# Kernel optimization log

Hardware: AMD Instinct MI355X
Metric: run time of the kernel (lower is better)

## Reference

```python
import jax, jax.numpy as jnp
import numpy as np

B, D, H = 16384, 1024, 4096


def setup_inputs() -> dict:
    key = jax.random.key(0)
    kx, kp, k1, k2 = jax.random.split(key, 4)
    X = jax.random.normal(kx, (B, D), dtype=jnp.float32)
    prot_col_idx = 3
    # protected column must be binary {0,1} so the remap produces no NaNs
    prot = jax.random.randint(kp, (B,), 0, 2).astype(jnp.float32)
    X = X.at[:, prot_col_idx].set(prot)
    W1 = jax.random.normal(k1, (D, H), dtype=jnp.float32) * (1.0 / np.sqrt(D))
    b1 = jnp.zeros((H,), dtype=jnp.float32)
    W2 = jax.random.normal(k2, (H, D), dtype=jnp.float32) * (1.0 / np.sqrt(H))
    b2 = jnp.zeros((D,), dtype=jnp.float32)
    return {"X": X, "W1": W1, "b1": b1, "W2": W2, "b2": b2,
            "prot_col_idx": prot_col_idx}


def reference(X, W1, b1, W2, b2, prot_col_idx):
    def explainer(x):
        h = jnp.tanh(x @ W1 + b1)          # [B, H]
        return h @ W2 + b2                  # [B, D]

    # vectorized remap of the protected column: 0 -> 1, 1 -> 0, else NaN
    col = X[:, prot_col_idx]
    flipped = jnp.where(col == 0, jnp.float32(1.0),
                        jnp.where(col == 1, jnp.float32(0.0), jnp.float32(jnp.nan)))
    X_copy = X.at[:, prot_col_idx].set(flipped.astype(X.dtype))

    shaps = explainer(X)
    shaps_counter = explainer(X_copy)
    mean_euclid_dist = jnp.mean(jnp.abs(shaps - shaps_counter), axis=0)  # [D]
    return mean_euclid_dist.sum()
```

## Files before the change

kernel.cpp:

```cpp
#include <hip/hip_runtime.h>
#include <stdint.h>

#define B_N 16384
#define D_N 1024
#define H_N 4096

typedef int i32x4 __attribute__((ext_vector_type(4)));
typedef int i32x8 __attribute__((ext_vector_type(8)));
typedef float f32x4 __attribute__((ext_vector_type(4)));

__device__ __forceinline__ void gload16(const void* g, void* l) {
  __builtin_amdgcn_global_load_lds((const __attribute__((address_space(1))) void*)g,
                                   (__attribute__((address_space(3))) void*)l,
                                   16, 0, 0);
}

__device__ __forceinline__ unsigned char f2fp8(float v) {
  return (unsigned char)(__builtin_amdgcn_cvt_pk_fp8_f32(v, v, 0, false) & 0xFF);
}

__device__ __forceinline__ int perm_h(int h) {
  return (h & ~63) | ((h & 15) << 2) | ((h >> 4) & 3);
}

__device__ __forceinline__ void transpose_tile(
    const float* __restrict__ in, unsigned char* __restrict__ out,
    int R, int C, float scale, float* __restrict__ w3, int pci,
    int i0, int j0, int tx, int ty, bool permute) {
  __shared__ float tile[32][33];
#pragma unroll
  for (int r = 0; r < 32; r += 8) {
    int i = i0 + ty + r;
    int j = j0 + tx;
    float v = in[(size_t)i * C + j];
    tile[ty + r][tx] = v;
    if (w3 != nullptr && i == pci) w3[j] = v;
  }
  __syncthreads();
#pragma unroll
  for (int r = 0; r < 32; r += 8) {
    int jo = j0 + ty + r;
    int io = i0 + tx;
    int ioo = permute ? perm_h(io) : io;
    out[(size_t)jo * R + ioo] = f2fp8(tile[tx][ty + r] * scale);
  }
}

__global__ __launch_bounds__(256) void prep_kernel(
    const float4* __restrict__ X4, int* __restrict__ Xb,
    float* __restrict__ s,
    const float* __restrict__ W1, unsigned char* __restrict__ W1T, float* __restrict__ w3,
    const float* __restrict__ W2, unsigned char* __restrict__ W2T,
    const int* __restrict__ pci_p, float* __restrict__ out0) {
  int b = blockIdx.x;
  int tid = threadIdx.x;
  int pci = *pci_p;
  if (b == 0 && tid == 0) out0[0] = 0.0f;
  if (b < 8192) {
    int i = (b * 256 + tid) * 2;
#pragma unroll
    for (int u = 0; u < 2; u++) {
      float4 v = X4[i + u];
      int p = __builtin_amdgcn_cvt_pk_fp8_f32(v.x, v.y, 0, false);
      p = __builtin_amdgcn_cvt_pk_fp8_f32(v.z, v.w, p, true);
      Xb[i + u] = p;
      if (((i + u) & (D_N / 4 - 1)) == (pci >> 2)) {
        int row = (i + u) >> 8;
        float c;
        switch (pci & 3) {
          case 0:  c = v.x; break;
          case 1:  c = v.y; break;
          case 2:  c = v.z; break;
          default: c = v.w; break;
        }
        s[row] = 1.0f - 2.0f * c;
      }
    }
  } else if (b < 12288) {
    int id = b - 8192;
    transpose_tile(W1, W1T, D_N, H_N, 16.0f, w3, pci,
                   (id >> 7) * 32, (id & 127) * 32, tid & 31, tid >> 5, false);
  } else {
    int id = b - 12288;
    transpose_tile(W2, W2T, H_N, D_N, 64.0f, nullptr, -1,
                   (id >> 5) * 32, (id & 31) * 32, tid & 31, tid >> 5, true);
  }
}

template <int KTOT>
__device__ __forceinline__ void mx8_mainloop(
    const unsigned char* __restrict__ A, const unsigned char* __restrict__ B,
    int m0, int n0, int sa, int sb,
    unsigned char* __restrict__ As, unsigned char* __restrict__ Bs,
    f32x4 (&acc)[8][4]) {
  static_assert(KTOT % 256 == 0, "need an even number of 128-K tiles");
  const int tid = threadIdx.x;
  const int lane = tid & 63;
  const int wave = tid >> 6;
  const int wm = (wave >> 2) * 128;
  const int wn = (wave & 3) * 64;
  const int lm = lane & 15;
  const int quad = lane >> 4;

  const int srow = tid >> 3;
  const int sg = tid & 7;
  const unsigned char* Ag = A + (size_t)(m0 + srow) * KTOT + ((sg ^ (srow & 7)) * 16);
  const unsigned char* Bg = B + (size_t)(n0 + srow) * KTOT + ((sg ^ (srow & 7)) * 16);
  unsigned char* AsW = As + tid * 16;
  unsigned char* BsW = Bs + tid * 16;

  const int e = lm & 7;
  const int lo_off = ((2 * quad) ^ e) * 16;
  const int hi_off = ((2 * quad + 1) ^ e) * 16;
  const unsigned char* Ard_lo = As + (wm + lm) * 128 + lo_off;
  const unsigned char* Ard_hi = As + (wm + lm) * 128 + hi_off;
  const unsigned char* Brd_lo = Bs + (wn + lm) * 128 + lo_off;
  const unsigned char* Brd_hi = Bs + (wn + lm) * 128 + hi_off;

  i32x8 bA0, bA1, bA2, bA3, bB0, bB1, bB2, bB3;
  i32x8 ax0, ax1, ay0, ay1;

#define STGA(c_, kn_, p_) \
    gload16(Ag + (kn_) + (size_t)(c_) * 64 * KTOT, AsW + (p_) * 32768 + (c_) * 8192)
#define STGB(c_, kn_, p_) \
    gload16(Bg + (kn_) + (size_t)(c_) * 64 * KTOT, BsW + (p_) * 32768 + (c_) * 8192)
#define LDA(d_, i_, P_) { \
    i32x4 lo_ = *(const i32x4*)(Ard_lo + (P_) * 32768 + (i_) * 2048); \
    i32x4 hi_ = *(const i32x4*)(Ard_hi + (P_) * 32768 + (i_) * 2048); \
    d_ = __builtin_shufflevector(lo_, hi_, 0, 1, 2, 3, 4, 5, 6, 7); }
#define LDB(d_, j_, P_) { \
    i32x4 lo_ = *(const i32x4*)(Brd_lo + (P_) * 32768 + (j_) * 2048); \
    i32x4 hi_ = *(const i32x4*)(Brd_hi + (P_) * 32768 + (j_) * 2048); \
    d_ = __builtin_shufflevector(lo_, hi_, 0, 1, 2, 3, 4, 5, 6, 7); }
#define MF(a_, b_, c_) \
    __builtin_amdgcn_mfma_scale_f32_16x16x128_f8f6f4((a_), (b_), (c_), 0, 0, 0, sa, 0, sb)
#define BARR() { asm volatile("" ::: "memory"); __builtin_amdgcn_s_barrier(); \
                 asm volatile("" ::: "memory"); }
#define VM(n_) asm volatile("s_waitcnt vmcnt(" #n_ ")" ::: "memory")
#define SCHED0() __builtin_amdgcn_sched_barrier(0)
#define MM8(i0_, i1_, aA_, aB_, B0_, B1_, B2_, B3_) { \
    __builtin_amdgcn_s_setprio(1); \
    acc[i0_][0] = MF(aA_, B0_, acc[i0_][0]); \
    acc[i0_][1] = MF(aA_, B1_, acc[i0_][1]); \
    acc[i0_][2] = MF(aA_, B2_, acc[i0_][2]); \
    acc[i0_][3] = MF(aA_, B3_, acc[i0_][3]); \
    acc[i1_][0] = MF(aB_, B0_, acc[i1_][0]); \
    acc[i1_][1] = MF(aB_, B1_, acc[i1_][1]); \
    acc[i1_][2] = MF(aB_, B2_, acc[i1_][2]); \
    acc[i1_][3] = MF(aB_, B3_, acc[i1_][3]); \
    __builtin_amdgcn_s_setprio(0); }

#define TILE(P_, BC0_, BC1_, BC2_, BC3_, BN0_, BN1_, BN2_, BN3_, kn_, LAST_) { \
     \
    LDA(ay0, 2, P_); LDA(ay1, 3, P_); \
    if (!(LAST_)) { STGB(0, kn_, 1 - (P_)); STGB(1, kn_, 1 - (P_)); } \
    SCHED0(); \
    MM8(0, 1, ax0, ax1, BC0_, BC1_, BC2_, BC3_); \
    if (LAST_) { VM(0); } else { VM(2); }   \
    BARR(); \
     \
    LDA(ax0, 4, P_); LDA(ax1, 5, P_); \
    if (!(LAST_)) { STGB(2, kn_, 1 - (P_)); STGB(3, kn_, 1 - (P_)); \
                    STGA(0, kn_, 1 - (P_)); STGA(2, kn_, 1 - (P_)); } \
    SCHED0(); \
    MM8(2, 3, ay0, ay1, BC0_, BC1_, BC2_, BC3_); \
    BARR(); \
     \
    LDA(ay0, 6, P_); LDA(ay1, 7, P_); \
    if (!(LAST_)) { STGA(1, kn_, 1 - (P_)); STGA(3, kn_, 1 - (P_)); } \
    SCHED0(); \
    MM8(4, 5, ax0, ax1, BC0_, BC1_, BC2_, BC3_); \
    if (!(LAST_)) { VM(2); }   \
    BARR(); \
     \
    if (!(LAST_)) { \
      LDB(BN0_, 0, 1 - (P_)); LDB(BN1_, 1, 1 - (P_)); \
      LDB(BN2_, 2, 1 - (P_)); LDB(BN3_, 3, 1 - (P_)); \
      LDA(ax0, 0, 1 - (P_)); LDA(ax1, 1, 1 - (P_)); \
    } \
    SCHED0(); \
    MM8(6, 7, ay0, ay1, BC0_, BC1_, BC2_, BC3_); \
    if (!(LAST_)) { BARR(); } \
  }

  STGB(0, 0, 0); STGB(1, 0, 0); STGB(2, 0, 0); STGB(3, 0, 0);
  STGA(0, 0, 0); STGA(2, 0, 0);
  STGA(1, 0, 0); STGA(3, 0, 0);
  VM(2);
  BARR();
  LDB(bA0, 0, 0); LDB(bA1, 1, 0); LDB(bA2, 2, 0); LDB(bA3, 3, 0);
  LDA(ax0, 0, 0); LDA(ax1, 1, 0);

  const int NT = KTOT / 128;
  for (int t = 0; t < NT - 2; t += 2) {
    TILE(0, bA0, bA1, bA2, bA3, bB0, bB1, bB2, bB3, (t + 1) * 128, false);
    TILE(1, bB0, bB1, bB2, bB3, bA0, bA1, bA2, bA3, (t + 2) * 128, false);
  }
  TILE(0, bA0, bA1, bA2, bA3, bB0, bB1, bB2, bB3, (NT - 1) * 128, false);
  TILE(1, bB0, bB1, bB2, bB3, bA0, bA1, bA2, bA3, 0, true);

#undef STGA
#undef STGB
#undef LDA
#undef LDB
#undef MF
#undef BARR
#undef VM
#undef SCHED0
#undef MM8
#undef TILE
}

__global__ __launch_bounds__(512, 2) void gemm1_dh(
    const unsigned char* __restrict__ Xb,
    const unsigned char* __restrict__ W1T,
    const float* __restrict__ b1,
    const float* __restrict__ w3,
    const float* __restrict__ s,
    unsigned int* __restrict__ Dh4) {
  __shared__ alignas(16) unsigned char As[65536];
  __shared__ alignas(16) unsigned char Bs[65536];
  const int l = blockIdx.x;
  const int x = l & 7;
  const int k = l >> 3;
  const int m0 = (x * 8 + (k & 7)) * 256;
  const int n0 = (k >> 3) * 256;

  f32x4 acc[8][4] = {};
  mx8_mainloop<D_N>(Xb, W1T, m0, n0, 127, 123, As, Bs, acc);

  const int tid = threadIdx.x;
  const int lane = tid & 63;
  const int wave = tid >> 6;
  const int wm = (wave >> 2) * 128;
  const int wn = (wave & 3) * 64;
  const int lm = lane & 15;
  const int quad = lane >> 4;

  float ewp[4], ewm[4], nump[4], numm[4], b1v[4];
#pragma unroll
  for (int j = 0; j < 4; j++) {
    int gh = n0 + wn + j * 16 + lm;
    float w = w3[gh];
    float ep = __expf(2.0f * w);
    float em = __expf(-2.0f * w);
    ewp[j] = ep; ewm[j] = em;
    nump[j] = 128.0f * (1.0f - ep);
    numm[j] = 128.0f * (1.0f - em);
    b1v[j] = b1[gh];
  }
  const size_t coloff = (size_t)((n0 + wn) >> 2) + lm;
#pragma unroll
  for (int i = 0; i < 8; i++) {
#pragma unroll
    for (int r = 0; r < 4; r++) {
      int gb = m0 + wm + i * 16 + quad * 4 + r;
      bool sp = s[gb] > 0.0f;
      float o[4];
#pragma unroll
      for (int j = 0; j < 4; j++) {
        float ews = sp ? ewp[j] : ewm[j];
        float num = sp ? nump[j] : numm[j];
        float z = fminf(acc[i][j][r] + b1v[j], 12.0f);
        float E = __expf(2.0f * z);
        float den = (E * ews + 1.0f) * (E + 1.0f);
        o[j] = (E * num) * __builtin_amdgcn_rcpf(den);
      }
      int p = __builtin_amdgcn_cvt_pk_fp8_f32(o[0], o[1], 0, false);
      p = __builtin_amdgcn_cvt_pk_fp8_f32(o[2], o[3], p, true);
      Dh4[(size_t)gb * (H_N / 4) + coloff] = (unsigned int)p;
    }
  }
}

__global__ __launch_bounds__(512, 2) void gemm2_abs(
    const unsigned char* __restrict__ Dh,
    const unsigned char* __restrict__ W2T,
    float* __restrict__ out) {
  __shared__ alignas(16) unsigned char As[65536];
  __shared__ alignas(16) unsigned char Bs[65536];
  __shared__ float wsum[8];
  const int l = blockIdx.x;
  const int x = l & 7;
  const int k = l >> 3;
  const int m0 = (x * 8 + (k & 7)) * 256;
  const int n0 = (k >> 3) * 256;

  f32x4 acc[8][4] = {};
  mx8_mainloop<H_N>(Dh, W2T, m0, n0, 121, 121, As, Bs, acc);

  const int tid = threadIdx.x;
  const int lane = tid & 63;
  const int wave = tid >> 6;

  float t = 0.0f;
#pragma unroll
  for (int i = 0; i < 8; i++)
#pragma unroll
    for (int j = 0; j < 4; j++)
#pragma unroll
      for (int r = 0; r < 4; r++)
        t += fabsf(acc[i][j][r]);

#pragma unroll
  for (int off2 = 32; off2 > 0; off2 >>= 1)
    t += __shfl_down(t, off2, 64);
  if (lane == 0) wsum[wave] = t;
  __syncthreads();
  if (tid == 0) {
    float tt = 0.0f;
#pragma unroll
    for (int w = 0; w < 8; w++) tt += wsum[w];
    atomicAdd(out, tt * (1.0f / (float)B_N));
  }
}

extern "C" void kernel_launch(void* const* d_in, const int* in_sizes, int n_in,
                              void* d_out, int out_size, void* d_ws, size_t ws_size,
                              hipStream_t stream) {
  const float* X  = (const float*)d_in[0];
  const float* W1 = (const float*)d_in[1];
  const float* b1 = (const float*)d_in[2];
  const float* W2 = (const float*)d_in[3];
  const int* pci  = (const int*)d_in[5];

  char* ws = (char*)d_ws;
  size_t off = 0;
  unsigned char* Xb  = (unsigned char*)(ws + off); off += (size_t)B_N * D_N;
  unsigned char* W1T = (unsigned char*)(ws + off); off += (size_t)H_N * D_N;
  unsigned char* W2T = (unsigned char*)(ws + off); off += (size_t)D_N * H_N;
  float* w3  = (float*)(ws + off); off += (size_t)H_N * 4;
  float* s   = (float*)(ws + off); off += (size_t)B_N * 4;
  unsigned char* Dh  = (unsigned char*)(ws + off); off += (size_t)B_N * H_N;
  if (ws_size < off) return;

  prep_kernel<<<16384, 256, 0, stream>>>((const float4*)X, (int*)Xb, s,
                                         W1, W1T, w3, W2, W2T, pci,
                                         (float*)d_out);
  gemm1_dh<<<1024, 512, 0, stream>>>(Xb, W1T, b1, w3, s, (unsigned int*)Dh);
  gemm2_abs<<<256, 512, 0, stream>>>(Dh, W2T, (float*)d_out);
}
```

Measured before the change: 275.3 us.

## Replace gemm1 256x256 pipelined mainloop with simple 128x128 tile kernel

The first GEMM (X·W1 with the tanh-difference epilogue) drops the 256x256, 512-thread, double-buffered and hand-scheduled mainloop. It now uses a simple 128x128, 256-thread kernel that is single-buffered with syncthreads around each K step and launches 4096 blocks in a 2D grid. The aim is more blocks per CU and a finer work split for this short-K (1024) GEMM. In exchange it loses load/compute overlap and halves data reuse per tile, which raises global and LDS traffic. gemm2 keeps the old pipelined loop.

```diff
diff --git a/kernel.cpp b/kernel.cpp
--- a/kernel.cpp
+++ b/kernel.cpp
@@ -84,6 +84,123 @@
     int id = b - 12288;
     transpose_tile(W2, W2T, H_N, D_N, 64.0f, nullptr, -1,
                    (id >> 5) * 32, (id & 31) * 32, tid & 31, tid >> 5, true);
+  }
+}
+
+template <int KTOT>
+__device__ __forceinline__ void mx_mainloop(
+    const unsigned char* __restrict__ A, const unsigned char* __restrict__ B,
+    int m0, int n0, int sa, int sb,
+    unsigned char* As, unsigned char* Bs, f32x4 (&acc)[4][4]) {
+  const int tid = threadIdx.x;
+  const int lane = tid & 63;
+  const int wave = tid >> 6;
+  const int wm = (wave >> 1) * 64;
+  const int wn = (wave & 1) * 64;
+  const int lm = lane & 15;
+  const int quad = lane >> 4;
+
+  const int srow = tid >> 3;
+  const int clog = (tid & 7) ^ (srow & 7);
+  const unsigned char* Ag = A + (size_t)(m0 + srow) * KTOT + clog * 16;
+  const unsigned char* Bg = B + (size_t)(n0 + srow) * KTOT + clog * 16;
+  unsigned char* As_l = As + tid * 16;
+  unsigned char* Bs_l = Bs + tid * 16;
+
+  for (int k0 = 0; k0 < KTOT; k0 += 128) {
+#pragma unroll
+    for (int it = 0; it < 4; it++) {
+      gload16(Ag + k0 + (size_t)(32 * it) * KTOT, As_l + it * 4096);
+      gload16(Bg + k0 + (size_t)(32 * it) * KTOT, Bs_l + it * 4096);
+    }
+    __syncthreads();
+    i32x8 b[4];
+#pragma unroll
+    for (int j = 0; j < 4; j++) {
+      int r = wn + j * 16 + lm;
+      int e = r & 7;
+      i32x4 lo = *(const i32x4*)&Bs[r * 128 + ((2 * quad) ^ e) * 16];
+      i32x4 hi = *(const i32x4*)&Bs[r * 128 + ((2 * quad + 1) ^ e) * 16];
+      b[j] = __builtin_shufflevector(lo, hi, 0, 1, 2, 3, 4, 5, 6, 7);
+    }
+#pragma unroll
+    for (int i = 0; i < 4; i++) {
+      int r = wm + i * 16 + lm;
+      int e = r & 7;
+      i32x4 lo = *(const i32x4*)&As[r * 128 + ((2 * quad) ^ e) * 16];
+      i32x4 hi = *(const i32x4*)&As[r * 128 + ((2 * quad + 1) ^ e) * 16];
+      i32x8 av = __builtin_shufflevector(lo, hi, 0, 1, 2, 3, 4, 5, 6, 7);
+#pragma unroll
+      for (int j = 0; j < 4; j++)
+        acc[i][j] = __builtin_amdgcn_mfma_scale_f32_16x16x128_f8f6f4(
+            av, b[j], acc[i][j], 0, 0, 0, sa, 0, sb);
+    }
+    __syncthreads();
+  }
+}
+
+__global__ __launch_bounds__(256, 4) void gemm1_dh(
+    const unsigned char* __restrict__ Xb,
+    const unsigned char* __restrict__ W1T,
+    const float* __restrict__ b1,
+    const float* __restrict__ w3,
+    const float* __restrict__ s,
+    unsigned int* __restrict__ Dh4) {
+  __shared__ alignas(16) unsigned char As[128 * 128];
+  __shared__ alignas(16) unsigned char Bs[128 * 128];
+  int l = blockIdx.y * gridDim.x + blockIdx.x;
+  int x = l & 7;
+  int k = l >> 3;
+  int ni = k & 7;
+  int m  = (k >> 3) & 15;
+  int nc = k >> 7;
+  const int m0 = (x * 16 + m) * 128;
+  const int n0 = (nc * 8 + ni) * 128;
+
+  f32x4 acc[4][4] = {};
+  mx_mainloop<D_N>(Xb, W1T, m0, n0, 127, 123, As, Bs, acc);
+
+  const int tid = threadIdx.x;
+  const int lane = tid & 63;
+  const int wave = tid >> 6;
+  const int wm = (wave >> 1) * 64;
+  const int wn = (wave & 1) * 64;
+  const int lm = lane & 15;
+  const int quad = lane >> 4;
+
+  float ewp[4], ewm[4], nump[4], numm[4], b1v[4];
+#pragma unroll
+  for (int j = 0; j < 4; j++) {
+    int gh = n0 + wn + j * 16 + lm;
+    float w = w3[gh];
+    float ep = __expf(2.0f * w);
+    float em = __expf(-2.0f * w);
+    ewp[j] = ep; ewm[j] = em;
+    nump[j] = 128.0f * (1.0f - ep);
+    numm[j] = 128.0f * (1.0f - em);
+    b1v[j] = b1[gh];
+  }
+  const size_t coloff = (size_t)((n0 + wn) >> 2) + lm;
+#pragma unroll
+  for (int i = 0; i < 4; i++) {
+#pragma unroll
+    for (int r = 0; r < 4; r++) {
+      int gb = m0 + wm + i * 16 + quad * 4 + r;
+      bool sp = s[gb] > 0.0f;
+      float o[4];
+#pragma unroll
+      for (int j = 0; j < 4; j++) {
+        float ews = sp ? ewp[j] : ewm[j];
+        float num = sp ? nump[j] : numm[j];
+        float z = fminf(acc[i][j][r] + b1v[j], 12.0f);
+        float E = __expf(2.0f * z);
+        float den = (E * ews + 1.0f) * (E + 1.0f);
+        o[j] = (E * num) * __builtin_amdgcn_rcpf(den);
+      }
+      int p = __builtin_amdgcn_cvt_pk_fp8_f32(o[0], o[1], 0, false);
+      p = __builtin_amdgcn_cvt_pk_fp8_f32(o[2], o[3], p, true);
+      Dh4[(size_t)gb * (H_N / 4) + coloff] = (unsigned int)p;
+    }
   }
 }
 
@@ -151,28 +268,24 @@
     __builtin_amdgcn_s_setprio(0); }
 
 #define TILE(P_, BC0_, BC1_, BC2_, BC3_, BN0_, BN1_, BN2_, BN3_, kn_, LAST_) { \
-     \
     LDA(ay0, 2, P_); LDA(ay1, 3, P_); \
     if (!(LAST_)) { STGB(0, kn_, 1 - (P_)); STGB(1, kn_, 1 - (P_)); } \
     SCHED0(); \
     MM8(0, 1, ax0, ax1, BC0_, BC1_, BC2_, BC3_); \
-    if (LAST_) { VM(0); } else { VM(2); }   \
+    if (LAST_) { VM(0); } else { VM(2); } \
     BARR(); \
-     \
     LDA(ax0, 4, P_); LDA(ax1, 5, P_); \
     if (!(LAST_)) { STGB(2, kn_, 1 - (P_)); STGB(3, kn_, 1 - (P_)); \
                     STGA(0, kn_, 1 - (P_)); STGA(2, kn_, 1 - (P_)); } \
     SCHED0(); \
     MM8(2, 3, ay0, ay1, BC0_, BC1_, BC2_, BC3_); \
     BARR(); \
-     \
     LDA(ay0, 6, P_); LDA(ay1, 7, P_); \
     if (!(LAST_)) { STGA(1, kn_, 1 - (P_)); STGA(3, kn_, 1 - (P_)); } \
     SCHED0(); \
     MM8(4, 5, ax0, ax1, BC0_, BC1_, BC2_, BC3_); \
-    if (!(LAST_)) { VM(2); }   \
+    if (!(LAST_)) { VM(2); } \
     BARR(); \
-     \
     if (!(LAST_)) { \
       LDB(BN0_, 0, 1 - (P_)); LDB(BN1_, 1, 1 - (P_)); \
       LDB(BN2_, 2, 1 - (P_)); LDB(BN3_, 3, 1 - (P_)); \
@@ -209,68 +322,6 @@
 #undef SCHED0
 #undef MM8
 #undef TILE
-}
-
-__global__ __launch_bounds__(512, 2) void gemm1_dh(
-    const unsigned char* __restrict__ Xb,
-    const unsigned char* __restrict__ W1T,
-    const float* __restrict__ b1,
-    const float* __restrict__ w3,
-    const float* __restrict__ s,
-    unsigned int* __restrict__ Dh4) {
-  __shared__ alignas(16) unsigned char As[65536];
-  __shared__ alignas(16) unsigned char Bs[65536];
-  const int l = blockIdx.x;
-  const int x = l & 7;
-  const int k = l >> 3;
-  const int m0 = (x * 8 + (k & 7)) * 256;
-  const int n0 = (k >> 3) * 256;
-
-  f32x4 acc[8][4] = {};
-  mx8_mainloop<D_N>(Xb, W1T, m0, n0, 127, 123, As, Bs, acc);
-
-  const int tid = threadIdx.x;
-  const int lane = tid & 63;
-  const int wave = tid >> 6;
-  const int wm = (wave >> 2) * 128;
-  const int wn = (wave & 3) * 64;
-  const int lm = lane & 15;
-  const int quad = lane >> 4;
-
-  float ewp[4], ewm[4], nump[4], numm[4], b1v[4];
-#pragma unroll
-  for (int j = 0; j < 4; j++) {
-    int gh = n0 + wn + j * 16 + lm;
-    float w = w3[gh];
-    float ep = __expf(2.0f * w);
-    float em = __expf(-2.0f * w);
-    ewp[j] = ep; ewm[j] = em;
-    nump[j] = 128.0f * (1.0f - ep);
-    numm[j] = 128.0f * (1.0f - em);
-    b1v[j] = b1[gh];
-  }
-  const size_t coloff = (size_t)((n0 + wn) >> 2) + lm;
-#pragma unroll
-  for (int i = 0; i < 8; i++) {
-#pragma unroll
-    for (int r = 0; r < 4; r++) {
-      int gb = m0 + wm + i * 16 + quad * 4 + r;
-      bool sp = s[gb] > 0.0f;
-      float o[4];
-#pragma unroll
-      for (int j = 0; j < 4; j++) {
-        float ews = sp ? ewp[j] : ewm[j];
-        float num = sp ? nump[j] : numm[j];
-        float z = fminf(acc[i][j][r] + b1v[j], 12.0f);
-        float E = __expf(2.0f * z);
-        float den = (E * ews + 1.0f) * (E + 1.0f);
-        o[j] = (E * num) * __builtin_amdgcn_rcpf(den);
-      }
-      int p = __builtin_amdgcn_cvt_pk_fp8_f32(o[0], o[1], 0, false);
-      p = __builtin_amdgcn_cvt_pk_fp8_f32(o[2], o[3], p, true);
-      Dh4[(size_t)gb * (H_N / 4) + coloff] = (unsigned int)p;
-    }
-  }
 }
 
 __global__ __launch_bounds__(512, 2) void gemm2_abs(
@@ -337,6 +388,7 @@
   prep_kernel<<<16384, 256, 0, stream>>>((const float4*)X, (int*)Xb, s,
                                          W1, W1T, w3, W2, W2T, pci,
                                          (float*)d_out);
-  gemm1_dh<<<1024, 512, 0, stream>>>(Xb, W1T, b1, w3, s, (unsigned int*)Dh);
+  gemm1_dh<<<dim3(32, 128), 256, 0, stream>>>(Xb, W1T, b1, w3, s,
+                                              (unsigned int*)Dh);
   gemm2_abs<<<256, 512, 0, stream>>>(Dh, W2T, (float*)d_out);
 }
```

After: 276.1 us. Within noise of the previous version (+0.3%).
